# Kernel tuning notes

Measured on AMD Instinct MI355X. Metric: run time of the kernel, lower is better.

The kernel has to match this reference:

```python
import jax, jax.numpy as jnp
import numpy as np

G, A = 1024, 20          # graphs, atoms per graph
N = G * A                # nodes = 20480
E = G * A * A            # fc edges within each graph = 409600
H = 128                  # hidden_dim
LATENT = 256             # latent_dim
L = 4                    # num_layers
NFREQ = 10
DIS_DIM = NFREQ * 2 * 3  # 60
EDGE_IN = 2 * H + 9 + DIS_DIM  # 325
MAX_ATOMS = 100


def _lin(k, fin, fout):
    return jax.random.normal(k, (fin, fout), dtype=jnp.float32) / np.sqrt(fin).astype(np.float32)


def _stack_lin(k, fin, fout):
    return jnp.stack([_lin(jax.random.fold_in(k, i), fin, fout) for i in range(L)])


def setup_inputs() -> dict:
    key = jax.random.key(0)
    ks = jax.random.split(key, 16)
    atom_types = jax.random.randint(ks[0], (N,), 0, MAX_ATOMS, dtype=jnp.int32)
    frac_coords = jax.random.uniform(ks[1], (N, 3), dtype=jnp.float32)
    lattices = jax.random.normal(ks[2], (G, 3, 3), dtype=jnp.float32)
    t = jax.random.normal(ks[3], (G, LATENT), dtype=jnp.float32)
    # fully-connected (fc) edges within each graph, block-diagonal structure
    base = np.arange(A)
    src = np.repeat(base, A)
    dst = np.tile(base, A)
    offs = (np.arange(G) * A)[:, None]
    edge_index = jnp.asarray(np.stack([
        (src[None, :] + offs).reshape(-1),
        (dst[None, :] + offs).reshape(-1)]), dtype=jnp.int32)  # [2, E]
    edge2graph = jnp.asarray(np.repeat(np.arange(G), A * A), dtype=jnp.int32)
    node2graph = jnp.asarray(np.repeat(np.arange(G), A), dtype=jnp.int32)
    # parameters
    emb_table = jax.random.normal(ks[4], (MAX_ATOMS, H), dtype=jnp.float32) * 0.02
    w_latent = _lin(ks[5], H + LATENT, H)
    b_latent = jnp.zeros((H,), jnp.float32)
    edge_w1 = _stack_lin(ks[6], EDGE_IN, H)
    edge_b1 = jnp.zeros((L, H), jnp.float32)
    edge_w2 = _stack_lin(ks[7], H, H)
    edge_b2 = jnp.zeros((L, H), jnp.float32)
    node_w1 = _stack_lin(ks[8], 2 * H, H)
    node_b1 = jnp.zeros((L, H), jnp.float32)
    node_w2 = _stack_lin(ks[9], H, H)
    node_b2 = jnp.zeros((L, H), jnp.float32)
    coord_w = _lin(ks[10], H, 3)
    lattice_w = _lin(ks[11], H, 9)
    return dict(atom_types=atom_types, frac_coords=frac_coords, lattices=lattices, t=t,
                edge_index=edge_index, edge2graph=edge2graph, node2graph=node2graph,
                emb_table=emb_table, w_latent=w_latent, b_latent=b_latent,
                edge_w1=edge_w1, edge_b1=edge_b1, edge_w2=edge_w2, edge_b2=edge_b2,
                node_w1=node_w1, node_b1=node_b1, node_w2=node_w2, node_b2=node_b2,
                coord_w=coord_w, lattice_w=lattice_w)


def reference(atom_types, frac_coords, lattices, t, edge_index, edge2graph, node2graph,
              emb_table, w_latent, b_latent,
              edge_w1, edge_b1, edge_w2, edge_b2,
              node_w1, node_b1, node_w2, node_b2,
              coord_w, lattice_w):
    silu = jax.nn.silu
    src, dst = edge_index[0], edge_index[1]
    # node embedding + latent conditioning
    h = emb_table[atom_types]                               # [N,H]
    h = jnp.concatenate([h, t[node2graph]], axis=1) @ w_latent + b_latent  # [N,H]
    # sinusoidal distance embedding of periodic frac diff (detached in original)
    frac_diff = (frac_coords[dst] - frac_coords[src]) % 1.0  # [E,3]
    freqs = 2.0 * jnp.pi * jnp.arange(NFREQ, dtype=frac_coords.dtype)
    emb = (frac_diff[..., None] * freqs).reshape(-1, 3 * NFREQ)
    dis = jax.lax.stop_gradient(jnp.concatenate([jnp.sin(emb), jnp.cos(emb)], axis=-1))  # [E,60]
    # lattice inner products, broadcast to edges (ip=True)
    lat_ip = jnp.einsum('gij,gkj->gik', lattices, lattices).reshape(-1, 9)
    lat_edges = lat_ip[edge2graph]                          # [E,9]
    # per-node edge counts for scatter-mean
    counts = jax.ops.segment_sum(jnp.ones_like(src, dtype=h.dtype), src, num_segments=N)
    inv_counts = (1.0 / jnp.maximum(counts, 1.0))[:, None]
    for i in range(L):
        e_in = jnp.concatenate([h[src], h[dst], lat_edges, dis], axis=1)  # [E,325]
        ef = silu(e_in @ edge_w1[i] + edge_b1[i])
        ef = silu(ef @ edge_w2[i] + edge_b2[i])               # [E,H]
        agg = jax.ops.segment_sum(ef, src, num_segments=N) * inv_counts   # scatter-mean
        n_in = jnp.concatenate([h, agg], axis=1)              # [N,2H]
        nf = silu(n_in @ node_w1[i] + node_b1[i])
        nf = silu(nf @ node_w2[i] + node_b2[i])
        h = h + nf                                            # residual
    coord_out = h @ coord_w                                   # [N,3]
    gcounts = jax.ops.segment_sum(jnp.ones((h.shape[0],), h.dtype), node2graph, num_segments=G)
    graph_feat = jax.ops.segment_sum(h, node2graph, num_segments=G) / gcounts[:, None]
    lattice_out = (graph_feat @ lattice_w).reshape(-1, 3, 3)
    lattice_out = jnp.einsum('bij,bjk->bik', lattice_out, lattices)  # ip=True
    return lattice_out, coord_out
```

## Files before the change

kernel.cpp:

```cpp
#include <hip/hip_runtime.h>
#include <stdint.h>


#define NA 20
#define HH 128

typedef unsigned short U16;
typedef unsigned int   U32;
typedef __attribute__((ext_vector_type(8))) short bf8;
typedef __attribute__((ext_vector_type(4))) float f4;

__device__ __forceinline__ float bf2f(U16 u){ return __uint_as_float(((U32)u)<<16); }
__device__ __forceinline__ U16 f2bf(float f){
    return (U16)((__float_as_uint(f) + 0x8000u) >> 16);
}
__device__ __forceinline__ float silu_f(float x){ return x/(1.0f+__expf(-x)); }
template<bool BF>
__device__ __forceinline__ float ldf(const void* p, long i){
    return BF ? bf2f(((const U16*)p)[i]) : ((const float*)p)[i];
}
__device__ __forceinline__ f4 mfma(bf8 a, bf8 b, f4 c){
    return __builtin_amdgcn_mfma_f32_16x16x32_bf16(a,b,c,0,0,0);
}
__device__ __forceinline__ bf8 ldsA(const U16* base, int stride, int row0,
                                    int kbase, int lrow, int quad){
    return *(const bf8*)(base + (row0+lrow)*stride + kbase + quad*8);
}
template<bool BF, bool WS>
__device__ __forceinline__ bf8 getB(const U16* wsb, long wbase, int kt, int nt,
                                    int lane, const void* W, long gbase, int N,
                                    int col, int kbase, int kmax, int quad){
    if constexpr(WS){
        return *(const bf8*)(wsb + wbase + (((long)kt*8 + nt)*64 + lane)*8);
    } else {
        bf8 b; int ks0 = kbase + quad*8;
#pragma unroll
        for(int j=0;j<8;j++){
            int k=ks0+j; U16 v=0;
            if(k<kmax) v = BF ? ((const U16*)W)[gbase+(long)k*N+col]
                              : f2bf(((const float*)W)[gbase+(long)k*N+col]);
            b[j]=(short)v;
        }
        return b;
    }
}

#define WS_LBASE(L) (49152 + (long)(L)*106496)
#define REPACK_BYTES 950272

__global__ __launch_bounds__(256) void repack(
    const void* wlat, const void* ew1, const void* ew2,
    const void* nw1p, const void* nw2p, const void* lat, U16* out)
{
    __shared__ int sG[4];
    const int tid=threadIdx.x;
    {
        const U16* l16=(const U16*)lat; int good=0;
#pragma unroll
        for(int u=0;u<32;u++){
            U16 x=l16[tid*32+u]; int e=(x>>7)&0xFF; good+=(e>=100&&e<=150)?1:0;
        }
#pragma unroll
        for(int o=32;o>0;o>>=1) good+=__shfl_xor(good,o);
        if((tid&63)==0) sG[tid>>6]=good;
    }
    __syncthreads();
    const bool bf = (sG[0]+sG[1]+sG[2]+sG[3]) > 6144;

    const void* W; long srow; int segk; long dst;
    const int ktg=blockIdx.x;
    if(ktg<12){ W=wlat; srow=(long)ktg*32; segk=32; dst=(long)ktg*4096; }
    else{
        int r=ktg-12, L=r/26, lk=r-26*L;
        dst = 49152 + (long)L*106496 + (long)lk*4096;
        if(lk<4)      { W=ew1;  srow=(long)L*325+lk*32;          segk=32; }
        else if(lk<8) { W=ew1;  srow=(long)L*325+128+(lk-4)*32;  segk=32; }
        else if(lk<10){ W=ew1;  srow=(long)L*325+265+(lk-8)*32;  segk=60-(lk-8)*32; }
        else if(lk<14){ W=ew2;  srow=(long)L*128+(lk-10)*32;     segk=32; }
        else if(lk<22){ W=nw1p; srow=(long)L*256+(lk-14)*32;     segk=32; }
        else          { W=nw2p; srow=(long)L*128+(lk-22)*32;     segk=32; }
    }
    for(int o=tid;o<4096;o+=256){
        int nt=o>>9, lane=(o>>3)&63, j=o&7;
        int kk=((lane>>4)<<3)+j, col=nt*16+(lane&15);
        U16 v=0;
        if(kk<segk){
            long idx=(srow+kk)*128+col;
            v = bf ? ((const U16*)W)[idx] : f2bf(((const float*)W)[idx]);
        }
        out[dst+o]=v;
    }
}

#define PB_OFF 8960
#define QB_OFF 11520
#define DB_OFF 14080
#define EB_OFF 19840

__device__ __forceinline__ void stage_dis(U16* dB, const float* tb, int ch, int tid){
    const float2* t2=(const float2*)tb;
#pragma unroll
    for(int it=0; it<5; ++it){
        int p = tid + it*512;
        int r = p>>5, j = p&31;
        if(j<30){
            int s = ch*4 + (r&3), d = r>>2;
            float2 vs = t2[s*30+j];
            float2 vd = t2[d*30+j];
            dB[r*72+j]    = f2bf(vd.x*vs.y - vd.y*vs.x);
            dB[r*72+j+30] = f2bf(vd.y*vs.y + vd.x*vs.x);
        }
    }
}

template<bool BF, bool WS>
__device__ void body(U16* sm, float* red, float* tb, const U16* wsb, int g, int tid,
    const int* __restrict__ atype, const void* frac, const void* lattices,
    const void* t, const void* emb, const void* wlat, const void* blat,
    const void* ew1, const void* eb1, const void* ew2, const void* eb2,
    const void* nw1p, const void* nb1, const void* nw2p, const void* nb2,
    const void* coordw, const void* latw, void* outv)
{
    const int lane=tid&63, w=tid>>6, lrow=lane&15, quad=lane>>4;
    const int c = w*16 + lrow;
    U16* HA=sm; U16* pB=sm+PB_OFF; U16* qB=sm+QB_OFF;
    U16* dB=sm+DB_OFF; U16* eB=sm+EB_OFF;
    U16* k1A=eB;
    float* tvecF=(float*)dB;

    for(int q=tid;q<8960;q+=512) HA[q]=0;
    for(int q=tid;q<32*136;q+=512){
        int n=q/136, cc=q-n*136; U16 v=0;
        if(n<20 && cc<128)
            v = BF ? ((const U16*)emb)[(long)atype[g*NA+n]*HH+cc]
                   : f2bf(((const float*)emb)[(long)atype[g*NA+n]*HH+cc]);
        k1A[q]=v;
    }
    for(int q=tid;q<600;q+=512){
        int n=q/30, jj=q-n*30;
        int dim=jj/10, f=jj-dim*10;
        float x = ldf<BF>(frac,(long)(g*NA+n)*3+dim);
        float rev = __builtin_amdgcn_fractf((float)f*x);
        float2 sc;
        sc.x=__builtin_amdgcn_sinf(rev);
        sc.y=__builtin_amdgcn_cosf(rev);
        ((float2*)tb)[q]=sc;
    }
    {
        int sl=tid>>7, j=tid&127; float acc=0.f;
        for(int kk=0;kk<64;kk++){
            int k=sl*64+kk;
            acc += ldf<BF>(t,(long)g*256+k)*ldf<BF>(wlat,(long)(HH+k)*HH+j);
        }
        tvecF[sl*128+j]=acc;
    }
    __syncthreads();
    {
        f4 a0={0.f,0.f,0.f,0.f}, a1={0.f,0.f,0.f,0.f};
#pragma unroll
        for(int ks=0;ks<4;ks++){
            bf8 b=getB<BF,WS>(wsb,0,ks,w,lane, wlat,0,HH,c,ks*32,128,quad);
            bf8 v0=ldsA(k1A,136,0,ks*32,lrow,quad);
            bf8 v1=ldsA(k1A,136,16,ks*32,lrow,quad);
            a0=mfma(v0,b,a0); a1=mfma(v1,b,a1);
        }
        float bias=ldf<BF>(blat,c)+tvecF[c]+tvecF[128+c]+tvecF[256+c]+tvecF[384+c];
#pragma unroll
        for(int r=0;r<4;r++){
            int r0=quad*4+r, r1=16+quad*4+r;
            if(r0<20) HA[r0*280+c]=f2bf(a0[r]+bias);
            if(r1<20) HA[r1*280+c]=f2bf(a1[r]+bias);
        }
    }
    __syncthreads();
    for(int q=tid;q<80*72;q+=512) dB[q]=0;

    for(int L=0;L<4;L++){
        const long e1=(long)L*325*HH;
        const long LB=WS_LBASE(L);
        if(tid<HH){
            float la[9];
#pragma unroll
            for(int m2=0;m2<9;m2++) la[m2]=ldf<BF>(lattices,(long)g*9+m2);
            float Rv=ldf<BF>(eb1,(long)L*HH+tid);
#pragma unroll
            for(int a2=0;a2<3;a2++)
#pragma unroll
            for(int b3=0;b3<3;b3++){
                float ip=0.f;
#pragma unroll
                for(int c2=0;c2<3;c2++) ip+=la[a2*3+c2]*la[b3*3+c2];
                Rv += ip*ldf<BF>(ew1, e1+(long)(256+a2*3+b3)*HH+tid);
            }
            red[tid]=Rv;
        }
        __syncthreads();
        {
            f4 p0={0.f,0.f,0.f,0.f}, p1={0.f,0.f,0.f,0.f};
#pragma unroll
            for(int ks=0;ks<4;ks++){
                bf8 b=getB<BF,WS>(wsb,LB,ks,w,lane, ew1,e1,HH,c,ks*32,128,quad);
                bf8 v0=ldsA(HA,280,0,ks*32,lrow,quad);
                bf8 v1=ldsA(HA,280,16,ks*32,lrow,quad);
                p0=mfma(v0,b,p0); p1=mfma(v1,b,p1);
            }
            float Rc=red[c];
#pragma unroll
            for(int r=0;r<4;r++){
                int r0=quad*4+r, r1=16+quad*4+r;
                if(r0<20) pB[r0*HH+c]=f2bf(p0[r]+Rc);
                if(r1<20) pB[r1*HH+c]=f2bf(p1[r]+Rc);
            }
        }
        {
            f4 q0={0.f,0.f,0.f,0.f}, q1={0.f,0.f,0.f,0.f};
#pragma unroll
            for(int ks=0;ks<4;ks++){
                bf8 b=getB<BF,WS>(wsb,LB+16384,ks,w,lane, ew1,e1+128*HH,HH,c,ks*32,128,quad);
                bf8 v0=ldsA(HA,280,0,ks*32,lrow,quad);
                bf8 v1=ldsA(HA,280,16,ks*32,lrow,quad);
                q0=mfma(v0,b,q0); q1=mfma(v1,b,q1);
            }
#pragma unroll
            for(int r=0;r<4;r++){
                int r0=quad*4+r, r1=16+quad*4+r;
                if(r0<20) qB[r0*HH+c]=f2bf(q0[r]);
                if(r1<20) qB[r1*HH+c]=f2bf(q1[r]);
            }
        }
        bf8 w1d0=getB<BF,WS>(wsb,LB+32768,0,w,lane, ew1,e1+(long)265*HH,HH,c,0, 60,quad);
        bf8 w1d1=getB<BF,WS>(wsb,LB+32768,1,w,lane, ew1,e1+(long)265*HH,HH,c,32,60,quad);
        bf8 w2f[4];
#pragma unroll
        for(int ks=0;ks<4;ks++)
            w2f[ks]=getB<BF,WS>(wsb,LB+40960,ks,w,lane, ew2,(long)L*HH*HH,HH,c,ks*32,128,quad);
        const float b2=ldf<BF>(eb2,(long)L*HH+c);
        stage_dis(dB,tb,0,tid);
        __syncthreads();

        for(int ch=0;ch<5;ch++){
            float pv[4];
#pragma unroll
            for(int r=0;r<4;r++) pv[r]=bf2f(pB[(ch*4+r)*HH+c]);
#pragma unroll
            for(int m=0;m<5;m++){
                f4 a={0.f,0.f,0.f,0.f};
                bf8 v0=ldsA(dB,72,m*16,0, lrow,quad);
                bf8 v1=ldsA(dB,72,m*16,32,lrow,quad);
                a=mfma(v0,w1d0,a); a=mfma(v1,w1d1,a);
                float qd=bf2f(qB[(m*4+quad)*HH+c]);
#pragma unroll
                for(int r=0;r<4;r++){
                    int row=m*16+quad*4+r;
                    eB[row*136+c]=f2bf(silu_f(a[r]+pv[r]+qd));
                }
            }
            __syncthreads();
            if(ch<4) stage_dis(dB,tb,ch+1,tid);
            float part[4]={0.f,0.f,0.f,0.f};
#pragma unroll
            for(int m=0;m<5;m++){
                f4 a={0.f,0.f,0.f,0.f};
#pragma unroll
                for(int ks=0;ks<4;ks++){
                    bf8 v=ldsA(eB,136,m*16,ks*32,lrow,quad);
                    a=mfma(v,w2f[ks],a);
                }
#pragma unroll
                for(int r=0;r<4;r++) part[r]+=silu_f(a[r]+b2);
            }
#pragma unroll
            for(int r=0;r<4;r++){
                float v=part[r];
                v+=__shfl_xor(v,16); v+=__shfl_xor(v,32);
                part[r]=v;
            }
            if(quad==0){
#pragma unroll
                for(int r=0;r<4;r++)
                    HA[(ch*4+r)*280+128+c]=f2bf(part[r]*0.05f);
            }
            __syncthreads();
        }
        {
            f4 a0={0.f,0.f,0.f,0.f}, a1={0.f,0.f,0.f,0.f};
#pragma unroll
            for(int ks=0;ks<8;ks++){
                bf8 b=getB<BF,WS>(wsb,LB+57344,ks,w,lane, nw1p,(long)L*256*HH,HH,c,ks*32,256,quad);
                bf8 v0=ldsA(HA,280,0,ks*32,lrow,quad);
                bf8 v1=ldsA(HA,280,16,ks*32,lrow,quad);
                a0=mfma(v0,b,a0); a1=mfma(v1,b,a1);
            }
            float n1=ldf<BF>(nb1,(long)L*HH+c);
#pragma unroll
            for(int r=0;r<4;r++){
                int r0=quad*4+r, r1=16+quad*4+r;
                eB[r0*136+c]=f2bf(r0<20 ? silu_f(a0[r]+n1) : 0.f);
                eB[r1*136+c]=f2bf(r1<20 ? silu_f(a1[r]+n1) : 0.f);
            }
        }
        __syncthreads();
        {
            f4 a0={0.f,0.f,0.f,0.f}, a1={0.f,0.f,0.f,0.f};
#pragma unroll
            for(int ks=0;ks<4;ks++){
                bf8 b=getB<BF,WS>(wsb,LB+90112,ks,w,lane, nw2p,(long)L*HH*HH,HH,c,ks*32,128,quad);
                bf8 v0=ldsA(eB,136,0,ks*32,lrow,quad);
                bf8 v1=ldsA(eB,136,16,ks*32,lrow,quad);
                a0=mfma(v0,b,a0); a1=mfma(v1,b,a1);
            }
            float n2=ldf<BF>(nb2,(long)L*HH+c);
#pragma unroll
            for(int r=0;r<4;r++){
                int r0=quad*4+r, r1=16+quad*4+r;
                if(r0<20) HA[r0*280+c]=f2bf(bf2f(HA[r0*280+c])+silu_f(a0[r]+n2));
                if(r1<20) HA[r1*280+c]=f2bf(bf2f(HA[r1*280+c])+silu_f(a1[r]+n2));
            }
        }
        __syncthreads();
    }

    {
        int o=tid>>3, l8=tid&7;
        float acc=0.f;
        int n=o/3, cc=o-n*3;
        if(o<60){
#pragma unroll
            for(int k8=0;k8<16;k8++){
                int k=l8*16+k8;
                acc += bf2f(HA[n*280+k]) * ldf<BF>(coordw,(long)k*3+cc);
            }
        }
        acc+=__shfl_xor(acc,1); acc+=__shfl_xor(acc,2); acc+=__shfl_xor(acc,4);
        if(o<60 && l8==0){
            if(BF) ((U16*)outv)[(long)1024*9+(long)(g*NA+n)*3+cc]=f2bf(acc);
            else   ((float*)outv)[(long)1024*9+(long)(g*NA+n)*3+cc]=acc;
        }
    }
    if(tid<HH){
        float s2=0.f;
        for(int n=0;n<NA;n++) s2+=bf2f(HA[n*280+tid]);
        red[tid]=s2*0.05f;
    }
    __syncthreads();
    {
        int o=tid>>4, l16=tid&15;
        float acc=0.f;
        if(o<9){
#pragma unroll
            for(int k8=0;k8<8;k8++){
                int k=l16*8+k8;
                acc += red[k]*ldf<BF>(latw,(long)k*9+o);
            }
        }
        acc+=__shfl_xor(acc,1); acc+=__shfl_xor(acc,2);
        acc+=__shfl_xor(acc,4); acc+=__shfl_xor(acc,8);
        if(o<9 && l16==0) red[HH+o]=acc;
    }
    __syncthreads();
    if(tid<9){
        int i2=tid/3, k2=tid-(tid/3)*3; float acc=0.f;
#pragma unroll
        for(int j3=0;j3<3;j3++)
            acc+=red[HH+i2*3+j3]*ldf<BF>(lattices,(long)g*9+j3*3+k2);
        if(BF) ((U16*)outv)[(long)g*9+tid]=f2bf(acc);
        else   ((float*)outv)[(long)g*9+tid]=acc;
    }
}

template<bool WS>
__device__ void mega_impl(const U16* wsb,
    const int* atype, const void* frac, const void* lattices, const void* t,
    const void* emb, const void* wlat, const void* blat,
    const void* ew1, const void* eb1, const void* ew2, const void* eb2,
    const void* nw1p, const void* nb1, const void* nw2p, const void* nb2,
    const void* coordw, const void* latw, void* outv)
{
    __shared__ __align__(16) unsigned char smraw[66880];
    U16* sm = (U16*)smraw;
    float* red = (float*)(smraw+61440);
    float* tb  = (float*)(smraw+62080);
    const int g=blockIdx.x, tid=threadIdx.x, w=tid>>6, lane=tid&63;
    int* di=(int*)red;
    {
        const U16* l16=(const U16*)lattices; int good=0;
#pragma unroll
        for(int u=0;u<16;u++){
            U16 x=l16[tid*16+u]; int e=(x>>7)&0xFF; good+=(e>=100&&e<=150)?1:0;
        }
#pragma unroll
        for(int o=32;o>0;o>>=1) good+=__shfl_xor(good,o);
        if(lane==0) di[w]=good;
    }
    __syncthreads();
    if(tid==0){ int s=0; for(int i=0;i<8;i++) s+=di[i]; di[8]=(s>6144)?1:0; }
    __syncthreads();
    const int bfm=di[8];
    __syncthreads();
    if(bfm) body<true ,WS>(sm,red,tb,wsb,g,tid,atype,frac,lattices,t,emb,wlat,blat,
                           ew1,eb1,ew2,eb2,nw1p,nb1,nw2p,nb2,coordw,latw,outv);
    else    body<false,WS>(sm,red,tb,wsb,g,tid,atype,frac,lattices,t,emb,wlat,blat,
                           ew1,eb1,ew2,eb2,nw1p,nb1,nw2p,nb2,coordw,latw,outv);
}

__global__ __launch_bounds__(512,2) void mega_ws(const U16* wsb,
    const int* atype, const void* frac, const void* lattices, const void* t,
    const void* emb, const void* wlat, const void* blat,
    const void* ew1, const void* eb1, const void* ew2, const void* eb2,
    const void* nw1p, const void* nb1, const void* nw2p, const void* nb2,
    const void* coordw, const void* latw, void* outv)
{
    mega_impl<true>(wsb,atype,frac,lattices,t,emb,wlat,blat,ew1,eb1,ew2,eb2,
                    nw1p,nb1,nw2p,nb2,coordw,latw,outv);
}

__global__ __launch_bounds__(512,2) void mega_direct(const U16* wsb,
    const int* atype, const void* frac, const void* lattices, const void* t,
    const void* emb, const void* wlat, const void* blat,
    const void* ew1, const void* eb1, const void* ew2, const void* eb2,
    const void* nw1p, const void* nb1, const void* nw2p, const void* nb2,
    const void* coordw, const void* latw, void* outv)
{
    mega_impl<false>(wsb,atype,frac,lattices,t,emb,wlat,blat,ew1,eb1,ew2,eb2,
                     nw1p,nb1,nw2p,nb2,coordw,latw,outv);
}

extern "C" void kernel_launch(void* const* d_in, const int* in_sizes, int n_in,
                              void* d_out, int out_size, void* d_ws, size_t ws_size,
                              hipStream_t stream)
{
    (void)in_sizes; (void)n_in; (void)out_size;
    const int* atype = (const int*)d_in[0];
    if(ws_size >= REPACK_BYTES){
        repack<<<116, 256, 0, stream>>>(d_in[8], d_in[10], d_in[12], d_in[14],
                                        d_in[16], d_in[2], (U16*)d_ws);
        mega_ws<<<1024, 512, 0, stream>>>((const U16*)d_ws,
            atype, d_in[1], d_in[2], d_in[3], d_in[7], d_in[8], d_in[9],
            d_in[10], d_in[11], d_in[12], d_in[13], d_in[14], d_in[15],
            d_in[16], d_in[17], d_in[18], d_in[19], d_out);
    } else {
        mega_direct<<<1024, 512, 0, stream>>>(nullptr,
            atype, d_in[1], d_in[2], d_in[3], d_in[7], d_in[8], d_in[9],
            d_in[10], d_in[11], d_in[12], d_in[13], d_in[14], d_in[15],
            d_in[16], d_in[17], d_in[18], d_in[19], d_out);
    }
}
```

Measured before the change: 398.3 us.

## Precompute per-layer lattice bias, fuse P/Q GEMMs, reuse dis tiles across layers, raise MFMA priority

```diff
diff --git a/kernel.cpp b/kernel.cpp
--- a/kernel.cpp
+++ b/kernel.cpp
@@ -114,7 +114,8 @@
 }
 
 template<bool BF, bool WS>
-__device__ void body(U16* sm, float* red, float* tb, const U16* wsb, int g, int tid,
+__device__ void body(U16* sm, float* red, float* tb, float* Rall,
+    const U16* wsb, int g, int tid,
     const int* __restrict__ atype, const void* frac, const void* lattices,
     const void* t, const void* emb, const void* wlat, const void* blat,
     const void* ew1, const void* eb1, const void* ew2, const void* eb2,
@@ -128,13 +129,10 @@
     U16* k1A=eB;
     float* tvecF=(float*)dB;
 
-    for(int q=tid;q<8960;q+=512) HA[q]=0;
-    for(int q=tid;q<32*136;q+=512){
-        int n=q/136, cc=q-n*136; U16 v=0;
-        if(n<20 && cc<128)
-            v = BF ? ((const U16*)emb)[(long)atype[g*NA+n]*HH+cc]
-                   : f2bf(((const float*)emb)[(long)atype[g*NA+n]*HH+cc]);
-        k1A[q]=v;
+    for(int q=tid;q<2560;q+=512){
+        int n=q>>7, cc=q&127;
+        k1A[n*136+cc] = BF ? ((const U16*)emb)[(long)atype[g*NA+n]*HH+cc]
+                           : f2bf(((const float*)emb)[(long)atype[g*NA+n]*HH+cc]);
     }
     for(int q=tid;q<600;q+=512){
         int n=q/30, jj=q-n*30;
@@ -154,6 +152,24 @@
         }
         tvecF[sl*128+j]=acc;
     }
+    {
+        int L=tid>>7, j=tid&127;
+        float la[9];
+#pragma unroll
+        for(int m2=0;m2<9;m2++) la[m2]=ldf<BF>(lattices,(long)g*9+m2);
+        float Rv=ldf<BF>(eb1,(long)L*HH+j);
+        const long e1=(long)L*325*HH;
+#pragma unroll
+        for(int a2=0;a2<3;a2++)
+#pragma unroll
+        for(int b3=0;b3<3;b3++){
+            float ip=0.f;
+#pragma unroll
+            for(int c2=0;c2<3;c2++) ip+=la[a2*3+c2]*la[b3*3+c2];
+            Rv += ip*ldf<BF>(ew1, e1+(long)(256+a2*3+b3)*HH+j);
+        }
+        Rall[L*128+j]=Rv;
+    }
     __syncthreads();
     {
         f4 a0={0.f,0.f,0.f,0.f}, a1={0.f,0.f,0.f,0.f};
@@ -167,65 +183,35 @@
         float bias=ldf<BF>(blat,c)+tvecF[c]+tvecF[128+c]+tvecF[256+c]+tvecF[384+c];
 #pragma unroll
         for(int r=0;r<4;r++){
-            int r0=quad*4+r, r1=16+quad*4+r;
-            if(r0<20) HA[r0*280+c]=f2bf(a0[r]+bias);
-            if(r1<20) HA[r1*280+c]=f2bf(a1[r]+bias);
-        }
-    }
-    __syncthreads();
-    for(int q=tid;q<80*72;q+=512) dB[q]=0;
+            HA[(quad*4+r)*280+c]   =f2bf(a0[r]+bias);
+            HA[(16+quad*4+r)*280+c]=f2bf(a1[r]+bias);
+        }
+    }
+    __syncthreads();
+    if(tid<320) dB[(tid>>2)*72+60+(tid&3)]=0;
 
     for(int L=0;L<4;L++){
         const long e1=(long)L*325*HH;
         const long LB=WS_LBASE(L);
-        if(tid<HH){
-            float la[9];
-#pragma unroll
-            for(int m2=0;m2<9;m2++) la[m2]=ldf<BF>(lattices,(long)g*9+m2);
-            float Rv=ldf<BF>(eb1,(long)L*HH+tid);
-#pragma unroll
-            for(int a2=0;a2<3;a2++)
-#pragma unroll
-            for(int b3=0;b3<3;b3++){
-                float ip=0.f;
-#pragma unroll
-                for(int c2=0;c2<3;c2++) ip+=la[a2*3+c2]*la[b3*3+c2];
-                Rv += ip*ldf<BF>(ew1, e1+(long)(256+a2*3+b3)*HH+tid);
-            }
-            red[tid]=Rv;
-        }
-        __syncthreads();
+        const int dir=L&1;
         {
             f4 p0={0.f,0.f,0.f,0.f}, p1={0.f,0.f,0.f,0.f};
+            f4 q0={0.f,0.f,0.f,0.f}, q1={0.f,0.f,0.f,0.f};
 #pragma unroll
             for(int ks=0;ks<4;ks++){
-                bf8 b=getB<BF,WS>(wsb,LB,ks,w,lane, ew1,e1,HH,c,ks*32,128,quad);
+                bf8 bp=getB<BF,WS>(wsb,LB,      ks,w,lane, ew1,e1,       HH,c,ks*32,128,quad);
+                bf8 bq=getB<BF,WS>(wsb,LB+16384,ks,w,lane, ew1,e1+128*HH,HH,c,ks*32,128,quad);
                 bf8 v0=ldsA(HA,280,0,ks*32,lrow,quad);
                 bf8 v1=ldsA(HA,280,16,ks*32,lrow,quad);
-                p0=mfma(v0,b,p0); p1=mfma(v1,b,p1);
-            }
-            float Rc=red[c];
+                p0=mfma(v0,bp,p0); p1=mfma(v1,bp,p1);
+                q0=mfma(v0,bq,q0); q1=mfma(v1,bq,q1);
+            }
+            float Rc=Rall[L*128+c];
 #pragma unroll
             for(int r=0;r<4;r++){
                 int r0=quad*4+r, r1=16+quad*4+r;
-                if(r0<20) pB[r0*HH+c]=f2bf(p0[r]+Rc);
-                if(r1<20) pB[r1*HH+c]=f2bf(p1[r]+Rc);
-            }
-        }
-        {
-            f4 q0={0.f,0.f,0.f,0.f}, q1={0.f,0.f,0.f,0.f};
-#pragma unroll
-            for(int ks=0;ks<4;ks++){
-                bf8 b=getB<BF,WS>(wsb,LB+16384,ks,w,lane, ew1,e1+128*HH,HH,c,ks*32,128,quad);
-                bf8 v0=ldsA(HA,280,0,ks*32,lrow,quad);
-                bf8 v1=ldsA(HA,280,16,ks*32,lrow,quad);
-                q0=mfma(v0,b,q0); q1=mfma(v1,b,q1);
-            }
-#pragma unroll
-            for(int r=0;r<4;r++){
-                int r0=quad*4+r, r1=16+quad*4+r;
-                if(r0<20) qB[r0*HH+c]=f2bf(q0[r]);
-                if(r1<20) qB[r1*HH+c]=f2bf(q1[r]);
+                if(r0<20){ pB[r0*HH+c]=f2bf(p0[r]+Rc); qB[r0*HH+c]=f2bf(q0[r]); }
+                if(r1<20){ pB[r1*HH+c]=f2bf(p1[r]+Rc); qB[r1*HH+c]=f2bf(q1[r]); }
             }
         }
         bf8 w1d0=getB<BF,WS>(wsb,LB+32768,0,w,lane, ew1,e1+(long)265*HH,HH,c,0, 60,quad);
@@ -235,19 +221,22 @@
         for(int ks=0;ks<4;ks++)
             w2f[ks]=getB<BF,WS>(wsb,LB+40960,ks,w,lane, ew2,(long)L*HH*HH,HH,c,ks*32,128,quad);
         const float b2=ldf<BF>(eb2,(long)L*HH+c);
-        stage_dis(dB,tb,0,tid);
+        if(L==0) stage_dis(dB,tb,0,tid);
         __syncthreads();
 
-        for(int ch=0;ch<5;ch++){
+        for(int i=0;i<5;i++){
+            const int ch = dir ? 4-i : i;
             float pv[4];
 #pragma unroll
             for(int r=0;r<4;r++) pv[r]=bf2f(pB[(ch*4+r)*HH+c]);
 #pragma unroll
             for(int m=0;m<5;m++){
                 f4 a={0.f,0.f,0.f,0.f};
+                __builtin_amdgcn_s_setprio(1);
                 bf8 v0=ldsA(dB,72,m*16,0, lrow,quad);
                 bf8 v1=ldsA(dB,72,m*16,32,lrow,quad);
                 a=mfma(v0,w1d0,a); a=mfma(v1,w1d1,a);
+                __builtin_amdgcn_s_setprio(0);
                 float qd=bf2f(qB[(m*4+quad)*HH+c]);
 #pragma unroll
                 for(int r=0;r<4;r++){
@@ -256,16 +245,18 @@
                 }
             }
             __syncthreads();
-            if(ch<4) stage_dis(dB,tb,ch+1,tid);
+            if(i<4) stage_dis(dB,tb, dir?3-i:i+1, tid);
             float part[4]={0.f,0.f,0.f,0.f};
 #pragma unroll
             for(int m=0;m<5;m++){
                 f4 a={0.f,0.f,0.f,0.f};
+                __builtin_amdgcn_s_setprio(1);
 #pragma unroll
                 for(int ks=0;ks<4;ks++){
                     bf8 v=ldsA(eB,136,m*16,ks*32,lrow,quad);
                     a=mfma(v,w2f[ks],a);
                 }
+                __builtin_amdgcn_s_setprio(0);
 #pragma unroll
                 for(int r=0;r<4;r++) part[r]+=silu_f(a[r]+b2);
             }
@@ -294,9 +285,8 @@
             float n1=ldf<BF>(nb1,(long)L*HH+c);
 #pragma unroll
             for(int r=0;r<4;r++){
-                int r0=quad*4+r, r1=16+quad*4+r;
-                eB[r0*136+c]=f2bf(r0<20 ? silu_f(a0[r]+n1) : 0.f);
-                eB[r1*136+c]=f2bf(r1<20 ? silu_f(a1[r]+n1) : 0.f);
+                eB[(quad*4+r)*136+c]   =f2bf(silu_f(a0[r]+n1));
+                eB[(16+quad*4+r)*136+c]=f2bf(silu_f(a1[r]+n1));
             }
         }
         __syncthreads();
@@ -313,8 +303,8 @@
 #pragma unroll
             for(int r=0;r<4;r++){
                 int r0=quad*4+r, r1=16+quad*4+r;
-                if(r0<20) HA[r0*280+c]=f2bf(bf2f(HA[r0*280+c])+silu_f(a0[r]+n2));
-                if(r1<20) HA[r1*280+c]=f2bf(bf2f(HA[r1*280+c])+silu_f(a1[r]+n2));
+                HA[r0*280+c]=f2bf(bf2f(HA[r0*280+c])+silu_f(a0[r]+n2));
+                HA[r1*280+c]=f2bf(bf2f(HA[r1*280+c])+silu_f(a1[r]+n2));
             }
         }
         __syncthreads();
@@ -376,10 +366,11 @@
     const void* nw1p, const void* nb1, const void* nw2p, const void* nb2,
     const void* coordw, const void* latw, void* outv)
 {
-    __shared__ __align__(16) unsigned char smraw[66880];
+    __shared__ __align__(16) unsigned char smraw[68928];
     U16* sm = (U16*)smraw;
     float* red = (float*)(smraw+61440);
     float* tb  = (float*)(smraw+62080);
+    float* Rall= (float*)(smraw+66880);
     const int g=blockIdx.x, tid=threadIdx.x, w=tid>>6, lane=tid&63;
     int* di=(int*)red;
     {
@@ -397,9 +388,9 @@
     __syncthreads();
     const int bfm=di[8];
     __syncthreads();
-    if(bfm) body<true ,WS>(sm,red,tb,wsb,g,tid,atype,frac,lattices,t,emb,wlat,blat,
+    if(bfm) body<true ,WS>(sm,red,tb,Rall,wsb,g,tid,atype,frac,lattices,t,emb,wlat,blat,
                            ew1,eb1,ew2,eb2,nw1p,nb1,nw2p,nb2,coordw,latw,outv);
-    else    body<false,WS>(sm,red,tb,wsb,g,tid,atype,frac,lattices,t,emb,wlat,blat,
+    else    body<false,WS>(sm,red,tb,Rall,wsb,g,tid,atype,frac,lattices,t,emb,wlat,blat,
                            ew1,eb1,ew2,eb2,nw1p,nb1,nw2p,nb2,coordw,latw,outv);
 }
 
```

New measurement: 397.3 us. About the same (-0.3%).
